# Kernel optimization log

Measured on AMD Instinct MI355X. Metric: run time of the kernel, lower is better.

The kernel has to match this reference:

```python
import jax, jax.numpy as jnp
import numpy as np

B, S, D, H = 2, 2048, 1024, 16
Dh = D // H
ROPE_BASE = 10000.0


def _rope_cos_sin(seq_len, dh, dtype):
    inv_freq = 1.0 / (ROPE_BASE ** (jnp.arange(0, dh, 2, dtype=jnp.float32) / dh))
    t = jnp.arange(seq_len, dtype=jnp.float32)
    freqs = jnp.outer(t, inv_freq)              # (S, Dh/2)
    emb = jnp.concatenate([freqs, freqs], -1)   # (S, Dh)
    return jnp.cos(emb).astype(dtype), jnp.sin(emb).astype(dtype)


def _rotate_half(x):
    x1, x2 = jnp.split(x, 2, axis=-1)
    return jnp.concatenate([-x2, x1], axis=-1)


def setup_inputs() -> dict:
    key = jax.random.key(0)
    k1, k2, k3 = jax.random.split(key, 3)
    x = jax.random.normal(k1, (B, S, D), dtype=jnp.float32)
    w_qkv = jax.random.normal(k2, (D, 3 * D), dtype=jnp.float32) * (1.0 / np.sqrt(D))
    w_proj = jax.random.normal(k3, (D, D), dtype=jnp.float32) * (1.0 / np.sqrt(D))
    return {"x": x, "w_qkv": w_qkv, "w_proj": w_proj}


def reference(x, w_qkv, w_proj):
    b, s, d = x.shape
    qkv = x @ w_qkv                              # (B, S, 3D)
    q, k, v = jnp.split(qkv, 3, axis=-1)
    # (B, S, D) -> (B, H, S, Dh)
    shape_heads = lambda t: t.reshape(b, s, H, Dh).transpose(0, 2, 1, 3)
    q, k, v = shape_heads(q), shape_heads(k), shape_heads(v)
    cos, sin = _rope_cos_sin(s, Dh, x.dtype)     # (S, Dh) each
    cos = cos[None, None]                        # (1,1,S,Dh)
    sin = sin[None, None]
    q = q * cos + _rotate_half(q) * sin
    k = k * cos + _rotate_half(k) * sin
    attn = jnp.einsum('bhqd,bhkd->bhqk', q, k) / np.sqrt(Dh).astype(x.dtype)
    causal_mask = jnp.tril(jnp.ones((s, s), dtype=bool))
    attn = jnp.where(causal_mask, attn, -jnp.inf)
    attn = jax.nn.softmax(attn, axis=-1)
    out = jnp.einsum('bhqk,bhkd->bhqd', attn, v)
    out = out.transpose(0, 2, 1, 3).reshape(b, s, d)
    return out @ w_proj
```

## Files before the change

kernel.cpp:

```cpp
#include <hip/hip_runtime.h>


typedef unsigned short u16;
typedef unsigned int u32;
typedef __bf16 bf16x8 __attribute__((ext_vector_type(8)));
typedef unsigned short u16x8 __attribute__((ext_vector_type(8)));
typedef unsigned short u16x4 __attribute__((ext_vector_type(4)));
typedef float f32x4 __attribute__((ext_vector_type(4)));

#define B_ 2
#define S_ 2048
#define D_ 1024
#define H_ 16
#define DH_ 64
#define BS_ (B_ * S_)
#define N3_ (3 * D_)

__device__ __forceinline__ u16 f2bf(float f) {
  unsigned u = __float_as_uint(f);
  u += 0x7FFFu + ((u >> 16) & 1u);
  return (u16)(u >> 16);
}
__device__ __forceinline__ float bf2f(u16 s) {
  return __uint_as_float(((unsigned)s) << 16);
}

union BU { u16x8 u; bf16x8 b; };

__device__ __forceinline__ void store_c(u16* C, size_t i, float v) { C[i] = f2bf(v); }
__device__ __forceinline__ void store_c(float* C, size_t i, float v) { C[i] = v; }

__device__ __forceinline__ void gl16(const void* g, void* l) {
  __builtin_amdgcn_global_load_lds(
      (const __attribute__((address_space(1))) u32*)g,
      (__attribute__((address_space(3))) u32*)l, 16, 0, 0);
}

__global__ __launch_bounds__(256) void k_cvt(const float* __restrict__ in,
                                             u16* __restrict__ out, int n4) {
  int i = blockIdx.x * 256 + threadIdx.x;
  if (i >= n4) return;
  const float4 f = ((const float4*)in)[i];
  u16x4 o;
  o[0] = f2bf(f.x); o[1] = f2bf(f.y); o[2] = f2bf(f.z); o[3] = f2bf(f.w);
  *(u16x4*)(out + (size_t)i * 4) = o;
}

__global__ __launch_bounds__(256) void k_cvt_T(const float* __restrict__ w,
                                               u16* __restrict__ wT, int R, int C) {
  __shared__ float tl[32][33];
  const int t = threadIdx.x;
  const int lrow = t >> 3, seg = t & 7;
  const int r0 = blockIdx.y * 32, c0 = blockIdx.x * 32;
  const float4 f = *(const float4*)(w + (size_t)(r0 + lrow) * C + c0 + seg * 4);
  tl[lrow][seg * 4 + 0] = f.x; tl[lrow][seg * 4 + 1] = f.y;
  tl[lrow][seg * 4 + 2] = f.z; tl[lrow][seg * 4 + 3] = f.w;
  __syncthreads();
  u16x4 o;
#pragma unroll
  for (int j = 0; j < 4; ++j) o[j] = f2bf(tl[seg * 4 + j][lrow]);
  *(u16x4*)(wT + (size_t)(c0 + lrow) * R + r0 + seg * 4) = o;
}

__global__ __launch_bounds__(256) void k_tab(float* __restrict__ ct, float* __restrict__ st) {
  const int idx = blockIdx.x * 256 + threadIdx.x;
  const int tpos = idx >> 5, i = idx & 31;
  const float invf = powf(10000.0f, -(float)i * (1.0f / 32.0f));
  const float a = (float)tpos * invf;
  ct[idx] = cosf(a);
  st[idx] = sinf(a);
}

template <typename OutT>
__global__ __launch_bounds__(256) void k_gemm(const u16* __restrict__ A,
                                              const u16* __restrict__ BT,
                                              OutT* __restrict__ C,
                                              int M, int N, int K) {
  __shared__ u16 la[2][128 * 32];
  __shared__ u16 lb[2][128 * 32];
  const int t = threadIdx.x;
  const int m0 = blockIdx.y * 128, n0 = blockIdx.x * 128;
  const int w = t >> 6, lane = t & 63;
  const int lr = lane & 15, lg = lane >> 4;
  const int wm = (w >> 1) * 64, wn = (w & 1) * 64;
  const int NK = K >> 5;

  const int srow = lane >> 2;
  const int sc = ((lane & 3) ^ ((lane >> 3) & 3)) * 8;
  const u16* Ag = A + (size_t)(m0 + w * 32 + srow) * K + sc;
  const u16* Bg = BT + (size_t)(n0 + w * 32 + srow) * K + sc;
  const int ldsw = w * 1024;

  f32x4 acc[4][4] = {};

#pragma unroll
  for (int i = 0; i < 2; ++i) {
    gl16(Ag + (size_t)i * 16 * K, la[0] + ldsw + i * 512);
    gl16(Bg + (size_t)i * 16 * K, lb[0] + ldsw + i * 512);
  }
  __syncthreads();

  int cur = 0;
  for (int kt = 0; kt < NK; ++kt) {
    if (kt + 1 < NK) {
      const int ko = (kt + 1) * 32;
#pragma unroll
      for (int i = 0; i < 2; ++i) {
        gl16(Ag + (size_t)i * 16 * K + ko, la[cur ^ 1] + ldsw + i * 512);
        gl16(Bg + (size_t)i * 16 * K + ko, lb[cur ^ 1] + ldsw + i * 512);
      }
    }
    const char* pa = (const char*)la[cur];
    const char* pb = (const char*)lb[cur];
    BU af[4], bfr[4];
    const int rsw = ((lr >> 1) & 3);
#pragma unroll
    for (int mi = 0; mi < 4; ++mi) {
      const int ra = wm + mi * 16 + lr;
      af[mi].u = *(const u16x8*)(pa + ra * 64 + ((lg ^ rsw) * 16));
      const int rb = wn + mi * 16 + lr;
      bfr[mi].u = *(const u16x8*)(pb + rb * 64 + ((lg ^ rsw) * 16));
    }
#pragma unroll
    for (int mi = 0; mi < 4; ++mi)
#pragma unroll
      for (int ni = 0; ni < 4; ++ni)
        acc[mi][ni] = __builtin_amdgcn_mfma_f32_16x16x32_bf16(af[mi].b, bfr[ni].b,
                                                              acc[mi][ni], 0, 0, 0);
    __syncthreads();
    cur ^= 1;
  }

#pragma unroll
  for (int mi = 0; mi < 4; ++mi)
#pragma unroll
    for (int ni = 0; ni < 4; ++ni)
#pragma unroll
      for (int r = 0; r < 4; ++r) {
        const int row = m0 + wm + mi * 16 + lg * 4 + r;
        const int col = n0 + wn + ni * 16 + lr;
        store_c(C, (size_t)row * N + col, acc[mi][ni][r]);
      }
}

__global__ __launch_bounds__(256) void k_prep(const u16* __restrict__ qkv,
                                              const float* __restrict__ ct,
                                              const float* __restrict__ st,
                                              u16* __restrict__ Q, u16* __restrict__ K,
                                              u16* __restrict__ Vt) {
  __shared__ u16 vl[64][72];
  const int stile = blockIdx.x, bh = blockIdx.y;
  const int b = bh >> 4, h = bh & 15;
  const int t = threadIdx.x;
  const int row = t >> 2, qr = t & 3;
  const int s = stile * 64 + row;
  const u16* base = qkv + (size_t)(b * S_ + s) * N3_ + h * DH_;
  const int d0 = qr * 8;
  float c[8], sn[8];
#pragma unroll
  for (int j = 0; j < 8; ++j) {
    c[j] = ct[s * 32 + d0 + j];
    sn[j] = st[s * 32 + d0 + j];
  }
#pragma unroll
  for (int part = 0; part < 2; ++part) {
    const float qs = (part == 0) ? 0.125f : 1.0f;
    const u16* src = base + part * D_;
    u16x8 lo = *(const u16x8*)(src + d0);
    u16x8 hi = *(const u16x8*)(src + d0 + 32);
    u16x8 olo, ohi;
#pragma unroll
    for (int j = 0; j < 8; ++j) {
      float x1 = bf2f(lo[j]) * qs, x2 = bf2f(hi[j]) * qs;
      olo[j] = f2bf(x1 * c[j] - x2 * sn[j]);
      ohi[j] = f2bf(x2 * c[j] + x1 * sn[j]);
    }
    u16* dst = (part ? K : Q) + ((size_t)bh * S_ + s) * DH_;
    *(u16x8*)(dst + d0) = olo;
    *(u16x8*)(dst + d0 + 32) = ohi;
  }
  u16x8 v0 = *(const u16x8*)(base + 2 * D_ + qr * 16);
  u16x8 v1 = *(const u16x8*)(base + 2 * D_ + qr * 16 + 8);
#pragma unroll
  for (int j = 0; j < 8; ++j) {
    vl[qr * 16 + j][row] = v0[j];
    vl[qr * 16 + 8 + j][row] = v1[j];
  }
  __syncthreads();
  const int dh = row, sc = qr * 16;
  u16x8 o0, o1;
#pragma unroll
  for (int j = 0; j < 8; ++j) { o0[j] = vl[dh][sc + j]; o1[j] = vl[dh][sc + 8 + j]; }
  u16* vdst = Vt + ((size_t)bh * DH_ + dh) * S_ + stile * 64 + sc;
  *(u16x8*)vdst = o0;
  *(u16x8*)(vdst + 8) = o1;
}

__global__ __launch_bounds__(256, 2) void k_attn(const u16* __restrict__ Q,
                                                 const u16* __restrict__ K,
                                                 const u16* __restrict__ Vt,
                                                 u16* __restrict__ Ao) {
  __shared__ char kvb_[2][16384];
  __shared__ char plb[4][2048];
  const int bid = blockIdx.x;
  const int xcd = bid & 7, inner = bid >> 3;
  const int bh = xcd + 8 * (inner & 3);
  const int f = inner >> 2;
  const int t = threadIdx.x;
  const int w = t >> 6, lane = t & 63;
  const int lr = lane & 15, lg = lane >> 4;

  const u16* Kbh = K + (size_t)bh * S_ * DH_;
  const u16* Vbh = Vt + (size_t)bh * DH_ * S_;

  const int sr = lane >> 3;
  const int sc = ((lane & 7) ^ sr) * 8;
  char* kd0 = kvb_[0] + w * 2048;
  char* kd1 = kvb_[1] + w * 2048;

  char* plw = plb[w];
  const int psw = (lr & 7) << 4;
  const int b = bh >> 4, h = bh & 15;

  for (int ph = 0; ph < 2; ++ph) {
    const int qt = ph ? 31 - f : f;
    const int q0 = qt * 64 + w * 16;
    const int nt = qt + 1;

    const u16* Qb = Q + ((size_t)bh * S_ + q0) * DH_;
    BU qf0, qf1;
    qf0.u = *(const u16x8*)(Qb + lr * DH_ + lg * 8);
    qf1.u = *(const u16x8*)(Qb + lr * DH_ + 32 + lg * 8);

    f32x4 o[4] = {};
    float m = -1e30f, l = 0.f;

    __syncthreads();
#pragma unroll
    for (int j = 0; j < 2; ++j) {
      const int row = w * 16 + j * 8 + sr;
      gl16(Kbh + (size_t)row * DH_ + sc, kd0 + j * 1024);
      gl16(Vbh + (size_t)row * S_ + sc, kd0 + 8192 + j * 1024);
    }
    __syncthreads();

    int cur = 0;
    for (int it = 0; it < nt; ++it) {
      const int kv0 = it * 64;
      if (it + 1 < nt) {
        const int kvn = kv0 + 64;
        char* nd = cur ? kd0 : kd1;
#pragma unroll
        for (int j = 0; j < 2; ++j) {
          const int row = w * 16 + j * 8 + sr;
          gl16(Kbh + (size_t)(kvn + row) * DH_ + sc, nd + j * 1024);
          gl16(Vbh + (size_t)row * S_ + kvn + sc, nd + 8192 + j * 1024);
        }
      }
      const char* base = kvb_[cur];
      f32x4 s[4] = {};
#pragma unroll
      for (int kvbi = 0; kvbi < 4; ++kvbi) {
        const int row = kvbi * 16 + lr;
        const int sw = (lr & 7) << 4;
        BU k0, k1;
        k0.u = *(const u16x8*)(base + row * 128 + ((lg * 16) ^ sw));
        k1.u = *(const u16x8*)(base + row * 128 + ((64 + lg * 16) ^ sw));
        s[kvbi] = __builtin_amdgcn_mfma_f32_16x16x32_bf16(k0.b, qf0.b, s[kvbi], 0, 0, 0);
        s[kvbi] = __builtin_amdgcn_mfma_f32_16x16x32_bf16(k1.b, qf1.b, s[kvbi], 0, 0, 0);
      }
      float p[16];
#pragma unroll
      for (int kvbi = 0; kvbi < 4; ++kvbi)
#pragma unroll
        for (int r = 0; r < 4; ++r) p[kvbi * 4 + r] = s[kvbi][r];
      if (it == nt - 1) {
#pragma unroll
        for (int kvbi = 0; kvbi < 4; ++kvbi)
#pragma unroll
          for (int r = 0; r < 4; ++r)
            if (kv0 + kvbi * 16 + lg * 4 + r > q0 + lr) p[kvbi * 4 + r] = -1e30f;
      }
      float mx = p[0];
#pragma unroll
      for (int i = 1; i < 16; ++i) mx = fmaxf(mx, p[i]);
      mx = fmaxf(mx, __shfl_xor(mx, 16, 64));
      mx = fmaxf(mx, __shfl_xor(mx, 32, 64));
      float al = 1.f;
      const bool resc = (mx > m + 8.f);
      if (resc) { al = __expf(m - mx); m = mx; }
      float sm = 0.f;
#pragma unroll
      for (int i = 0; i < 16; ++i) { p[i] = __expf(p[i] - m); sm += p[i]; }
      sm += __shfl_xor(sm, 16, 64);
      sm += __shfl_xor(sm, 32, 64);
      l = l * al + sm;
      if (resc) {
#pragma unroll
        for (int d = 0; d < 4; ++d)
#pragma unroll
          for (int r = 0; r < 4; ++r) o[d][r] *= al;
      }
#pragma unroll
      for (int kvbi = 0; kvbi < 4; ++kvbi) {
        u16x4 w4;
#pragma unroll
        for (int r = 0; r < 4; ++r) w4[r] = f2bf(p[kvbi * 4 + r]);
        *(u16x4*)(plw + lr * 128 + ((kvbi * 32 + lg * 8) ^ psw)) = w4;
      }
      BU pf0, pf1;
      pf0.u = *(const u16x8*)(plw + lr * 128 + ((lg * 16) ^ psw));
      pf1.u = *(const u16x8*)(plw + lr * 128 + ((64 + lg * 16) ^ psw));
#pragma unroll
      for (int d = 0; d < 4; ++d) {
        const int row = d * 16 + lr;
        const int sw = (lr & 7) << 4;
        BU v0, v1;
        v0.u = *(const u16x8*)(base + 8192 + row * 128 + ((lg * 16) ^ sw));
        v1.u = *(const u16x8*)(base + 8192 + row * 128 + ((64 + lg * 16) ^ sw));
        o[d] = __builtin_amdgcn_mfma_f32_16x16x32_bf16(v0.b, pf0.b, o[d], 0, 0, 0);
        o[d] = __builtin_amdgcn_mfma_f32_16x16x32_bf16(v1.b, pf1.b, o[d], 0, 0, 0);
      }
      __syncthreads();
      cur ^= 1;
    }

    const float inv = 1.0f / l;
    const size_t rowo = ((size_t)b * S_ + q0 + lr) * D_ + h * DH_;
#pragma unroll
    for (int d = 0; d < 4; ++d) {
      u16x4 w4;
#pragma unroll
      for (int r = 0; r < 4; ++r) w4[r] = f2bf(o[d][r] * inv);
      *(u16x4*)(Ao + rowo + d * 16 + lg * 4) = w4;
    }
  }
}

extern "C" void kernel_launch(void* const* d_in, const int* in_sizes, int n_in,
                              void* d_out, int out_size, void* d_ws, size_t ws_size,
                              hipStream_t stream) {
  const float* x = (const float*)d_in[0];
  const float* wqkv = (const float*)d_in[1];
  const float* wproj = (const float*)d_in[2];
  float* out = (float*)d_out;
  char* ws = (char*)d_ws;

  u16* xb      = (u16*)(ws + 0);
  u16* wqkvT   = (u16*)(ws + 8388608);
  u16* wprojT  = (u16*)(ws + 14680064);
  u16* qkvb    = (u16*)(ws + 16777216);
  u16* Qb      = (u16*)(ws + 41943040);
  u16* Kb      = (u16*)(ws + 50331648);
  u16* Vtb     = (u16*)(ws + 58720256);
  u16* aob     = (u16*)(ws + 67108864);
  float* ct    = (float*)(ws + 75497472);
  float* stab  = (float*)(ws + 75759616);

  k_cvt<<<4096, 256, 0, stream>>>(x, xb, BS_ * D_ / 4);
  k_cvt_T<<<dim3(96, 32), 256, 0, stream>>>(wqkv, wqkvT, D_, N3_);
  k_cvt_T<<<dim3(32, 32), 256, 0, stream>>>(wproj, wprojT, D_, D_);
  k_tab<<<256, 256, 0, stream>>>(ct, stab);

  k_gemm<u16><<<dim3(24, 32), 256, 0, stream>>>(xb, wqkvT, qkvb, BS_, N3_, D_);
  k_prep<<<dim3(32, 32), 256, 0, stream>>>(qkvb, ct, stab, Qb, Kb, Vtb);
  k_attn<<<512, 256, 0, stream>>>(Qb, Kb, Vtb, aob);
  k_gemm<float><<<dim3(8, 32), 256, 0, stream>>>(aob, wprojT, out, BS_, D_, D_);
}
```

Measured before the change: 131.2 us.

## Merge prep kernels, remap blocks per XCD, stage bf16 GEMM epilogue, split attention

Folds the x conversion, both weight transposes and the RoPE table build into one launch. GEMM and prep blocks are remapped so neighbouring tiles land on the same XCD, and the bf16 GEMM output goes through LDS so it can be written as 16-byte rows. Attention drops the paired short-plus-long query tile per block and launches one block per query tile, longest first. This cuts launch overhead and improves L2 locality and store coalescing, but the longest-first ordering may balance the causal work less evenly than the pairing did.

```diff
diff --git a/kernel.cpp b/kernel.cpp
--- a/kernel.cpp
+++ b/kernel.cpp
@@ -27,59 +27,74 @@
 
 union BU { u16x8 u; bf16x8 b; };
 
-__device__ __forceinline__ void store_c(u16* C, size_t i, float v) { C[i] = f2bf(v); }
-__device__ __forceinline__ void store_c(float* C, size_t i, float v) { C[i] = v; }
-
 __device__ __forceinline__ void gl16(const void* g, void* l) {
   __builtin_amdgcn_global_load_lds(
       (const __attribute__((address_space(1))) u32*)g,
       (__attribute__((address_space(3))) u32*)l, 16, 0, 0);
 }
 
-__global__ __launch_bounds__(256) void k_cvt(const float* __restrict__ in,
-                                             u16* __restrict__ out, int n4) {
-  int i = blockIdx.x * 256 + threadIdx.x;
-  if (i >= n4) return;
-  const float4 f = ((const float4*)in)[i];
-  u16x4 o;
-  o[0] = f2bf(f.x); o[1] = f2bf(f.y); o[2] = f2bf(f.z); o[3] = f2bf(f.w);
-  *(u16x4*)(out + (size_t)i * 4) = o;
-}
-
-__global__ __launch_bounds__(256) void k_cvt_T(const float* __restrict__ w,
-                                               u16* __restrict__ wT, int R, int C) {
+__global__ __launch_bounds__(256) void k_pre(const float* __restrict__ x,
+                                             const float* __restrict__ wqkv,
+                                             const float* __restrict__ wproj,
+                                             u16* __restrict__ xb,
+                                             u16* __restrict__ wqkvT,
+                                             u16* __restrict__ wprojT,
+                                             float* __restrict__ ct,
+                                             float* __restrict__ st) {
   __shared__ float tl[32][33];
+  const int bid = blockIdx.x;
   const int t = threadIdx.x;
-  const int lrow = t >> 3, seg = t & 7;
-  const int r0 = blockIdx.y * 32, c0 = blockIdx.x * 32;
-  const float4 f = *(const float4*)(w + (size_t)(r0 + lrow) * C + c0 + seg * 4);
-  tl[lrow][seg * 4 + 0] = f.x; tl[lrow][seg * 4 + 1] = f.y;
-  tl[lrow][seg * 4 + 2] = f.z; tl[lrow][seg * 4 + 3] = f.w;
-  __syncthreads();
-  u16x4 o;
-#pragma unroll
-  for (int j = 0; j < 4; ++j) o[j] = f2bf(tl[seg * 4 + j][lrow]);
-  *(u16x4*)(wT + (size_t)(c0 + lrow) * R + r0 + seg * 4) = o;
-}
-
-__global__ __launch_bounds__(256) void k_tab(float* __restrict__ ct, float* __restrict__ st) {
-  const int idx = blockIdx.x * 256 + threadIdx.x;
-  const int tpos = idx >> 5, i = idx & 31;
-  const float invf = powf(10000.0f, -(float)i * (1.0f / 32.0f));
-  const float a = (float)tpos * invf;
-  ct[idx] = cosf(a);
-  st[idx] = sinf(a);
+  if (bid < 4096) {
+    const int i = bid * 256 + t;
+    const float4 f = ((const float4*)x)[i];
+    u16x4 o;
+    o[0] = f2bf(f.x); o[1] = f2bf(f.y); o[2] = f2bf(f.z); o[3] = f2bf(f.w);
+    *(u16x4*)(xb + (size_t)i * 4) = o;
+    return;
+  }
+  if (bid < 8192) {
+    const float* w; u16* wT; int R, C, bx, by;
+    if (bid < 7168) {
+      w = wqkv; wT = wqkvT; R = D_; C = N3_;
+      const int id2 = bid - 4096; bx = id2 % 96; by = id2 / 96;
+    } else {
+      w = wproj; wT = wprojT; R = D_; C = D_;
+      const int id2 = bid - 7168; bx = id2 % 32; by = id2 / 32;
+    }
+    const int lrow = t >> 3, seg = t & 7;
+    const int r0 = by * 32, c0 = bx * 32;
+    const float4 f = *(const float4*)(w + (size_t)(r0 + lrow) * C + c0 + seg * 4);
+    tl[lrow][seg * 4 + 0] = f.x; tl[lrow][seg * 4 + 1] = f.y;
+    tl[lrow][seg * 4 + 2] = f.z; tl[lrow][seg * 4 + 3] = f.w;
+    __syncthreads();
+    u16x4 o;
+#pragma unroll
+    for (int j = 0; j < 4; ++j) o[j] = f2bf(tl[seg * 4 + j][lrow]);
+    *(u16x4*)(wT + (size_t)(c0 + lrow) * R + r0 + seg * 4) = o;
+    return;
+  }
+  {
+    const int idx = (bid - 8192) * 256 + t;
+    const int tpos = idx >> 5, i = idx & 31;
+    const float invf = powf(10000.0f, -(float)i * (1.0f / 32.0f));
+    const float a = (float)tpos * invf;
+    ct[idx] = cosf(a);
+    st[idx] = sinf(a);
+  }
 }
 
 template <typename OutT>
 __global__ __launch_bounds__(256) void k_gemm(const u16* __restrict__ A,
                                               const u16* __restrict__ BT,
                                               OutT* __restrict__ C,
-                                              int M, int N, int K) {
-  __shared__ u16 la[2][128 * 32];
-  __shared__ u16 lb[2][128 * 32];
+                                              int M, int N, int K, int nbx) {
+  __shared__ u16 smem[16384];
+  u16* laA = smem;
+  u16* laB = smem + 8192;
   const int t = threadIdx.x;
-  const int m0 = blockIdx.y * 128, n0 = blockIdx.x * 128;
+  const int per_x = gridDim.x >> 3;
+  const int nid = (blockIdx.x & 7) * per_x + (blockIdx.x >> 3);
+  const int n0 = (nid % nbx) * 128, m0 = (nid / nbx) * 128;
   const int w = t >> 6, lane = t & 63;
   const int lr = lane & 15, lg = lane >> 4;
   const int wm = (w >> 1) * 64, wn = (w & 1) * 64;
@@ -95,8 +110,8 @@
 
 #pragma unroll
   for (int i = 0; i < 2; ++i) {
-    gl16(Ag + (size_t)i * 16 * K, la[0] + ldsw + i * 512);
-    gl16(Bg + (size_t)i * 16 * K, lb[0] + ldsw + i * 512);
+    gl16(Ag + (size_t)i * 16 * K, laA + ldsw + i * 512);
+    gl16(Bg + (size_t)i * 16 * K, laB + ldsw + i * 512);
   }
   __syncthreads();
 
@@ -106,12 +121,12 @@
       const int ko = (kt + 1) * 32;
 #pragma unroll
       for (int i = 0; i < 2; ++i) {
-        gl16(Ag + (size_t)i * 16 * K + ko, la[cur ^ 1] + ldsw + i * 512);
-        gl16(Bg + (size_t)i * 16 * K + ko, lb[cur ^ 1] + ldsw + i * 512);
+        gl16(Ag + (size_t)i * 16 * K + ko, laA + (cur ^ 1) * 4096 + ldsw + i * 512);
+        gl16(Bg + (size_t)i * 16 * K + ko, laB + (cur ^ 1) * 4096 + ldsw + i * 512);
       }
     }
-    const char* pa = (const char*)la[cur];
-    const char* pb = (const char*)lb[cur];
+    const char* pa = (const char*)(laA + cur * 4096);
+    const char* pb = (const char*)(laB + cur * 4096);
     BU af[4], bfr[4];
     const int rsw = ((lr >> 1) & 3);
 #pragma unroll
@@ -131,16 +146,34 @@
     cur ^= 1;
   }
 
-#pragma unroll
-  for (int mi = 0; mi < 4; ++mi)
-#pragma unroll
-    for (int ni = 0; ni < 4; ++ni)
-#pragma unroll
-      for (int r = 0; r < 4; ++r) {
-        const int row = m0 + wm + mi * 16 + lg * 4 + r;
-        const int col = n0 + wn + ni * 16 + lr;
-        store_c(C, (size_t)row * N + col, acc[mi][ni][r]);
-      }
+  if constexpr (sizeof(OutT) == 2) {
+    u16* ew = smem + w * 4096;
+#pragma unroll
+    for (int mi = 0; mi < 4; ++mi)
+#pragma unroll
+      for (int ni = 0; ni < 4; ++ni)
+#pragma unroll
+        for (int r = 0; r < 4; ++r)
+          ew[(mi * 16 + lg * 4 + r) * 64 + ni * 16 + lr] = f2bf(acc[mi][ni][r]);
+    const int er = lane >> 3, es = (lane & 7) * 8;
+#pragma unroll
+    for (int pass = 0; pass < 8; ++pass) {
+      const int row = pass * 8 + er;
+      const u16x8 v = *(const u16x8*)(ew + row * 64 + es);
+      *(u16x8*)((u16*)C + (size_t)(m0 + wm + row) * N + n0 + wn + es) = v;
+    }
+  } else {
+#pragma unroll
+    for (int mi = 0; mi < 4; ++mi)
+#pragma unroll
+      for (int ni = 0; ni < 4; ++ni)
+#pragma unroll
+        for (int r = 0; r < 4; ++r) {
+          const int row = m0 + wm + mi * 16 + lg * 4 + r;
+          const int col = n0 + wn + ni * 16 + lr;
+          ((float*)C)[(size_t)row * N + col] = acc[mi][ni][r];
+        }
+  }
 }
 
 __global__ __launch_bounds__(256) void k_prep(const u16* __restrict__ qkv,
@@ -149,7 +182,10 @@
                                               u16* __restrict__ Q, u16* __restrict__ K,
                                               u16* __restrict__ Vt) {
   __shared__ u16 vl[64][72];
-  const int stile = blockIdx.x, bh = blockIdx.y;
+  const int bid = blockIdx.x;
+  const int xcd = bid & 7, slot = bid >> 3;
+  const int bh = xcd + 8 * (slot >> 5);
+  const int stile = slot & 31;
   const int b = bh >> 4, h = bh & 15;
   const int t = threadIdx.x;
   const int row = t >> 2, qr = t & 3;
@@ -205,10 +241,12 @@
   const int bid = blockIdx.x;
   const int xcd = bid & 7, inner = bid >> 3;
   const int bh = xcd + 8 * (inner & 3);
-  const int f = inner >> 2;
+  const int qt = 31 - (inner >> 2);
   const int t = threadIdx.x;
   const int w = t >> 6, lane = t & 63;
   const int lr = lane & 15, lg = lane >> 4;
+  const int q0 = qt * 64 + w * 16;
+  const int nt = qt + 1;
 
   const u16* Kbh = K + (size_t)bh * S_ * DH_;
   const u16* Vbh = Vt + (size_t)bh * DH_ * S_;
@@ -218,122 +256,114 @@
   char* kd0 = kvb_[0] + w * 2048;
   char* kd1 = kvb_[1] + w * 2048;
 
+  const u16* Qb = Q + ((size_t)bh * S_ + q0) * DH_;
+  BU qf0, qf1;
+  qf0.u = *(const u16x8*)(Qb + lr * DH_ + lg * 8);
+  qf1.u = *(const u16x8*)(Qb + lr * DH_ + 32 + lg * 8);
+
+  f32x4 o[4] = {};
+  float m = -1e30f, l = 0.f;
   char* plw = plb[w];
   const int psw = (lr & 7) << 4;
+
+#pragma unroll
+  for (int j = 0; j < 2; ++j) {
+    const int row = w * 16 + j * 8 + sr;
+    gl16(Kbh + (size_t)row * DH_ + sc, kd0 + j * 1024);
+    gl16(Vbh + (size_t)row * S_ + sc, kd0 + 8192 + j * 1024);
+  }
+  __syncthreads();
+
+  int cur = 0;
+  for (int it = 0; it < nt; ++it) {
+    const int kv0 = it * 64;
+    if (it + 1 < nt) {
+      const int kvn = kv0 + 64;
+      char* nd = cur ? kd0 : kd1;
+#pragma unroll
+      for (int j = 0; j < 2; ++j) {
+        const int row = w * 16 + j * 8 + sr;
+        gl16(Kbh + (size_t)(kvn + row) * DH_ + sc, nd + j * 1024);
+        gl16(Vbh + (size_t)row * S_ + kvn + sc, nd + 8192 + j * 1024);
+      }
+    }
+    const char* base = kvb_[cur];
+    f32x4 s[4] = {};
+#pragma unroll
+    for (int kvbi = 0; kvbi < 4; ++kvbi) {
+      const int row = kvbi * 16 + lr;
+      const int sw = (lr & 7) << 4;
+      BU k0, k1;
+      k0.u = *(const u16x8*)(base + row * 128 + ((lg * 16) ^ sw));
+      k1.u = *(const u16x8*)(base + row * 128 + ((64 + lg * 16) ^ sw));
+      s[kvbi] = __builtin_amdgcn_mfma_f32_16x16x32_bf16(k0.b, qf0.b, s[kvbi], 0, 0, 0);
+      s[kvbi] = __builtin_amdgcn_mfma_f32_16x16x32_bf16(k1.b, qf1.b, s[kvbi], 0, 0, 0);
+    }
+    float p[16];
+#pragma unroll
+    for (int kvbi = 0; kvbi < 4; ++kvbi)
+#pragma unroll
+      for (int r = 0; r < 4; ++r) p[kvbi * 4 + r] = s[kvbi][r];
+    if (it == nt - 1) {
+#pragma unroll
+      for (int kvbi = 0; kvbi < 4; ++kvbi)
+#pragma unroll
+        for (int r = 0; r < 4; ++r)
+          if (kv0 + kvbi * 16 + lg * 4 + r > q0 + lr) p[kvbi * 4 + r] = -1e30f;
+    }
+    float mx = p[0];
+#pragma unroll
+    for (int i = 1; i < 16; ++i) mx = fmaxf(mx, p[i]);
+    mx = fmaxf(mx, __shfl_xor(mx, 16, 64));
+    mx = fmaxf(mx, __shfl_xor(mx, 32, 64));
+    float al = 1.f;
+    const bool resc = (mx > m + 8.f);
+    if (resc) { al = __expf(m - mx); m = mx; }
+    float sm = 0.f;
+#pragma unroll
+    for (int i = 0; i < 16; ++i) { p[i] = __expf(p[i] - m); sm += p[i]; }
+    sm += __shfl_xor(sm, 16, 64);
+    sm += __shfl_xor(sm, 32, 64);
+    l = l * al + sm;
+    if (resc) {
+#pragma unroll
+      for (int d = 0; d < 4; ++d)
+#pragma unroll
+        for (int r = 0; r < 4; ++r) o[d][r] *= al;
+    }
+#pragma unroll
+    for (int kvbi = 0; kvbi < 4; ++kvbi) {
+      u16x4 w4;
+#pragma unroll
+      for (int r = 0; r < 4; ++r) w4[r] = f2bf(p[kvbi * 4 + r]);
+      *(u16x4*)(plw + lr * 128 + ((kvbi * 32 + lg * 8) ^ psw)) = w4;
+    }
+    BU pf0, pf1;
+    pf0.u = *(const u16x8*)(plw + lr * 128 + ((lg * 16) ^ psw));
+    pf1.u = *(const u16x8*)(plw + lr * 128 + ((64 + lg * 16) ^ psw));
+#pragma unroll
+    for (int d = 0; d < 4; ++d) {
+      const int row = d * 16 + lr;
+      const int sw = (lr & 7) << 4;
+      BU v0, v1;
+      v0.u = *(const u16x8*)(base + 8192 + row * 128 + ((lg * 16) ^ sw));
+      v1.u = *(const u16x8*)(base + 8192 + row * 128 + ((64 + lg * 16) ^ sw));
+      o[d] = __builtin_amdgcn_mfma_f32_16x16x32_bf16(v0.b, pf0.b, o[d], 0, 0, 0);
+      o[d] = __builtin_amdgcn_mfma_f32_16x16x32_bf16(v1.b, pf1.b, o[d], 0, 0, 0);
+    }
+    __syncthreads();
+    cur ^= 1;
+  }
+
+  const float inv = 1.0f / l;
   const int b = bh >> 4, h = bh & 15;
-
-  for (int ph = 0; ph < 2; ++ph) {
-    const int qt = ph ? 31 - f : f;
-    const int q0 = qt * 64 + w * 16;
-    const int nt = qt + 1;
-
-    const u16* Qb = Q + ((size_t)bh * S_ + q0) * DH_;
-    BU qf0, qf1;
-    qf0.u = *(const u16x8*)(Qb + lr * DH_ + lg * 8);
-    qf1.u = *(const u16x8*)(Qb + lr * DH_ + 32 + lg * 8);
-
-    f32x4 o[4] = {};
-    float m = -1e30f, l = 0.f;
-
-    __syncthreads();
-#pragma unroll
-    for (int j = 0; j < 2; ++j) {
-      const int row = w * 16 + j * 8 + sr;
-      gl16(Kbh + (size_t)row * DH_ + sc, kd0 + j * 1024);
-      gl16(Vbh + (size_t)row * S_ + sc, kd0 + 8192 + j * 1024);
-    }
-    __syncthreads();
-
-    int cur = 0;
-    for (int it = 0; it < nt; ++it) {
-      const int kv0 = it * 64;
-      if (it + 1 < nt) {
-        const int kvn = kv0 + 64;
-        char* nd = cur ? kd0 : kd1;
-#pragma unroll
-        for (int j = 0; j < 2; ++j) {
-          const int row = w * 16 + j * 8 + sr;
-          gl16(Kbh + (size_t)(kvn + row) * DH_ + sc, nd + j * 1024);
-          gl16(Vbh + (size_t)row * S_ + kvn + sc, nd + 8192 + j * 1024);
-        }
-      }
-      const char* base = kvb_[cur];
-      f32x4 s[4] = {};
-#pragma unroll
-      for (int kvbi = 0; kvbi < 4; ++kvbi) {
-        const int row = kvbi * 16 + lr;
-        const int sw = (lr & 7) << 4;
-        BU k0, k1;
-        k0.u = *(const u16x8*)(base + row * 128 + ((lg * 16) ^ sw));
-        k1.u = *(const u16x8*)(base + row * 128 + ((64 + lg * 16) ^ sw));
-        s[kvbi] = __builtin_amdgcn_mfma_f32_16x16x32_bf16(k0.b, qf0.b, s[kvbi], 0, 0, 0);
-        s[kvbi] = __builtin_amdgcn_mfma_f32_16x16x32_bf16(k1.b, qf1.b, s[kvbi], 0, 0, 0);
-      }
-      float p[16];
-#pragma unroll
-      for (int kvbi = 0; kvbi < 4; ++kvbi)
-#pragma unroll
-        for (int r = 0; r < 4; ++r) p[kvbi * 4 + r] = s[kvbi][r];
-      if (it == nt - 1) {
-#pragma unroll
-        for (int kvbi = 0; kvbi < 4; ++kvbi)
-#pragma unroll
-          for (int r = 0; r < 4; ++r)
-            if (kv0 + kvbi * 16 + lg * 4 + r > q0 + lr) p[kvbi * 4 + r] = -1e30f;
-      }
-      float mx = p[0];
-#pragma unroll
-      for (int i = 1; i < 16; ++i) mx = fmaxf(mx, p[i]);
-      mx = fmaxf(mx, __shfl_xor(mx, 16, 64));
-      mx = fmaxf(mx, __shfl_xor(mx, 32, 64));
-      float al = 1.f;
-      const bool resc = (mx > m + 8.f);
-      if (resc) { al = __expf(m - mx); m = mx; }
-      float sm = 0.f;
-#pragma unroll
-      for (int i = 0; i < 16; ++i) { p[i] = __expf(p[i] - m); sm += p[i]; }
-      sm += __shfl_xor(sm, 16, 64);
-      sm += __shfl_xor(sm, 32, 64);
-      l = l * al + sm;
-      if (resc) {
-#pragma unroll
-        for (int d = 0; d < 4; ++d)
-#pragma unroll
-          for (int r = 0; r < 4; ++r) o[d][r] *= al;
-      }
-#pragma unroll
-      for (int kvbi = 0; kvbi < 4; ++kvbi) {
-        u16x4 w4;
-#pragma unroll
-        for (int r = 0; r < 4; ++r) w4[r] = f2bf(p[kvbi * 4 + r]);
-        *(u16x4*)(plw + lr * 128 + ((kvbi * 32 + lg * 8) ^ psw)) = w4;
-      }
-      BU pf0, pf1;
-      pf0.u = *(const u16x8*)(plw + lr * 128 + ((lg * 16) ^ psw));
-      pf1.u = *(const u16x8*)(plw + lr * 128 + ((64 + lg * 16) ^ psw));
-#pragma unroll
-      for (int d = 0; d < 4; ++d) {
-        const int row = d * 16 + lr;
-        const int sw = (lr & 7) << 4;
-        BU v0, v1;
-        v0.u = *(const u16x8*)(base + 8192 + row * 128 + ((lg * 16) ^ sw));
-        v1.u = *(const u16x8*)(base + 8192 + row * 128 + ((64 + lg * 16) ^ sw));
-        o[d] = __builtin_amdgcn_mfma_f32_16x16x32_bf16(v0.b, pf0.b, o[d], 0, 0, 0);
-        o[d] = __builtin_amdgcn_mfma_f32_16x16x32_bf16(v1.b, pf1.b, o[d], 0, 0, 0);
-      }
-      __syncthreads();
-      cur ^= 1;
-    }
-
-    const float inv = 1.0f / l;
-    const size_t rowo = ((size_t)b * S_ + q0 + lr) * D_ + h * DH_;
-#pragma unroll
-    for (int d = 0; d < 4; ++d) {
-      u16x4 w4;
-#pragma unroll
-      for (int r = 0; r < 4; ++r) w4[r] = f2bf(o[d][r] * inv);
-      *(u16x4*)(Ao + rowo + d * 16 + lg * 4) = w4;
-    }
+  const size_t rowo = ((size_t)b * S_ + q0 + lr) * D_ + h * DH_;
+#pragma unroll
+  for (int d = 0; d < 4; ++d) {
+    u16x4 w4;
+#pragma unroll
+    for (int r = 0; r < 4; ++r) w4[r] = f2bf(o[d][r] * inv);
+    *(u16x4*)(Ao + rowo + d * 16 + lg * 4) = w4;
   }
 }
 
@@ -357,13 +387,9 @@
   float* ct    = (float*)(ws + 75497472);
   float* stab  = (float*)(ws + 75759616);
 
-  k_cvt<<<4096, 256, 0, stream>>>(x, xb, BS_ * D_ / 4);
-  k_cvt_T<<<dim3(96, 32), 256, 0, stream>>>(wqkv, wqkvT, D_, N3_);
-  k_cvt_T<<<dim3(32, 32), 256, 0, stream>>>(wproj, wprojT, D_, D_);
-  k_tab<<<256, 256, 0, stream>>>(ct, stab);
-
-  k_gemm<u16><<<dim3(24, 32), 256, 0, stream>>>(xb, wqkvT, qkvb, BS_, N3_, D_);
-  k_prep<<<dim3(32, 32), 256, 0, stream>>>(qkvb, ct, stab, Qb, Kb, Vtb);
-  k_attn<<<512, 256, 0, stream>>>(Qb, Kb, Vtb, aob);
-  k_gemm<float><<<dim3(8, 32), 256, 0, stream>>>(aob, wprojT, out, BS_, D_, D_);
-}
+  k_pre<<<8448, 256, 0, stream>>>(x, wqkv, wproj, xb, wqkvT, wprojT, ct, stab);
+  k_gemm<u16><<<768, 256, 0, stream>>>(xb, wqkvT, qkvb, BS_, N3_, D_, 24);
+  k_prep<<<1024, 256, 0, stream>>>(qkvb, ct, stab, Qb, Kb, Vtb);
+  k_attn<<<1024, 256, 0, stream>>>(Qb, Kb, Vtb, aob);
+  k_gemm<float><<<256, 256, 0, stream>>>(aob, wprojT, out, BS_, D_, D_, 8);
+}
```

New measurement: 119.4 us. 9.0% less time.
